# Optimization experiments

Hardware: AMD Instinct MI355X
Metric: run time of the kernel (lower is better)

The kernel has to match this reference:

```python
import jax, jax.numpy as jnp
import numpy as np


def deform_conv2d(x, w, offset, mask, pad):
    """Modulated deformable conv (DCNv2), stride 1, dilation 1, groups 1.
    x: [B,C,H,W], w: [Co,C,kh,kw], offset: [B,2*K,H,W] (y,x per tap), mask: [B,K,H,W].
    Output spatial size equals input (pad = (k-1)//2).
    """
    B, C, H, W = x.shape
    Co, _, kh, kw = w.shape
    K = kh * kw
    off = offset.reshape(B, K, 2, H, W)
    dy, dx = off[:, :, 0], off[:, :, 1]               # [B,K,H,W]
    ky, kx = jnp.meshgrid(jnp.arange(kh), jnp.arange(kw), indexing='ij')
    ky = ky.reshape(K).astype(x.dtype)
    kx = kx.reshape(K).astype(x.dtype)
    hh = jnp.arange(H, dtype=x.dtype)
    ww = jnp.arange(W, dtype=x.dtype)
    # sampling coords: p0 + p_k + delta p_k
    py = hh[None, None, :, None] - pad + ky[None, :, None, None] + dy  # [B,K,H,W]
    px = ww[None, None, None, :] - pad + kx[None, :, None, None] + dx
    y0 = jnp.floor(py)
    x0 = jnp.floor(px)
    wy = py - y0
    wx = px - x0
    y0i = y0.astype(jnp.int32)
    x0i = x0.astype(jnp.int32)
    x_flat = x.reshape(B, C, H * W)

    def gather(yi, xi):
        valid = (yi >= 0) & (yi < H) & (xi >= 0) & (xi < W)  # zero padding outside
        idx = jnp.clip(yi, 0, H - 1) * W + jnp.clip(xi, 0, W - 1)
        g = jnp.take_along_axis(x_flat, idx.reshape(B, 1, K * H * W), axis=2)
        g = g.reshape(B, C, K, H, W)
        return g * valid[:, None].astype(x.dtype)

    v00 = gather(y0i, x0i)
    v01 = gather(y0i, x0i + 1)
    v10 = gather(y0i + 1, x0i)
    v11 = gather(y0i + 1, x0i + 1)
    wy_ = wy[:, None]  # [B,1,K,H,W]
    wx_ = wx[:, None]
    samp = (v00 * (1 - wy_) * (1 - wx_) + v01 * (1 - wy_) * wx_
            + v10 * wy_ * (1 - wx_) + v11 * wy_ * wx_)   # [B,C,K,H,W]
    # masked weighted accumulation == conv over sampled taps
    return jnp.einsum('bckhw,bkhw,ock->bohw', samp, mask, w.reshape(Co, C, K))


def setup_inputs() -> dict:
    key = jax.random.key(0)
    ks = jax.random.split(key, 10)
    B, C, H, W, Co = 4, 64, 64, 64, 64
    inp = {
        'x': jax.random.normal(ks[0], (B, C, H, W), dtype=jnp.float32),
        'filter1': jax.random.normal(ks[1], (Co, C, 3, 3), dtype=jnp.float32) * 0.05,
        'offset1': jax.random.normal(ks[2], (B, 2 * 9, H, W), dtype=jnp.float32),
        'mask1': jax.random.uniform(ks[3], (B, 9, H, W), dtype=jnp.float32),
        'filter2': jax.random.normal(ks[4], (Co, C, 5, 5), dtype=jnp.float32) * 0.03,
        'offset2': jax.random.normal(ks[5], (B, 2 * 25, H, W), dtype=jnp.float32),
        'mask2': jax.random.uniform(ks[6], (B, 25, H, W), dtype=jnp.float32),
        'filter3': jax.random.normal(ks[7], (Co, C, 7, 7), dtype=jnp.float32) * 0.02,
        'offset3': jax.random.normal(ks[8], (B, 2 * 49, H, W), dtype=jnp.float32),
        'mask3': jax.random.uniform(ks[9], (B, 49, H, W), dtype=jnp.float32),
    }
    return inp


def reference(x, filter1, offset1, mask1, filter2, offset2, mask2, filter3, offset3, mask3):
    part1 = deform_conv2d(x, filter1, offset1, mask1, pad=1)  # 3x3
    part2 = deform_conv2d(x, filter2, offset2, mask2, pad=2)  # 5x5
    part3 = deform_conv2d(x, filter3, offset3, mask3, pad=3)  # 7x7
    return jnp.concatenate((part1, part2, part3), axis=1)
```

## Files before the change

### kernel.cpp

```cpp
#include <hip/hip_runtime.h>
#include <hip/hip_bf16.h>


typedef __attribute__((ext_vector_type(8))) short bf16x8;
typedef __attribute__((ext_vector_type(8))) unsigned short u16x8;
typedef __attribute__((ext_vector_type(4))) float f32x4;
typedef __attribute__((ext_vector_type(2))) float f32x2;

#define WR 16
#define WC 30
#define WS 68
#define SLS 20

__device__ __forceinline__ unsigned short f2bf(float f) {
    __hip_bfloat16 h = __float2bfloat16(f);
    return *reinterpret_cast<unsigned short*>(&h);
}
__device__ __forceinline__ f32x2 unpk(unsigned u) {
    f32x2 r;
    r[0] = __uint_as_float(u << 16);
    r[1] = __uint_as_float(u & 0xffff0000u);
    return r;
}

__global__ __launch_bounds__(256) void k_prep(
    const float* __restrict__ x,
    const float* __restrict__ f1, const float* __restrict__ f2, const float* __restrict__ f3,
    unsigned short* __restrict__ xTb,
    unsigned short* __restrict__ wp1, unsigned short* __restrict__ wp2, unsigned short* __restrict__ wp3) {
    __shared__ float tile[64][65];
    int bid = blockIdx.x;
    int tid = threadIdx.x;
    if (bid < 256) {
        int b = bid >> 6, h = bid & 63;
        {
            int w = tid & 63, c4 = tid >> 6;
            const float* xp = x + (((b * 64) * 64 + h) * 64) + w;
            #pragma unroll
            for (int i = 0; i < 16; ++i) {
                int c = c4 * 16 + i;
                tile[c][w] = xp[c * 4096];
            }
        }
        __syncthreads();
        {
            int c = tid & 63, w4 = tid >> 6;
            unsigned short* op = xTb + (((b * 64 + h) * 64) * 64) + c;
            #pragma unroll
            for (int i = 0; i < 16; ++i) {
                int ww = w4 * 16 + i;
                op[ww * 64] = f2bf(tile[c][ww]);
            }
        }
    } else {
        int idx = (bid - 256) * 256 + tid;
        const float* f; unsigned short* wp; int K, rel;
        if (idx < 36864)       { f = f1; wp = wp1; K = 9;  rel = idx; }
        else if (idx < 139264) { f = f2; wp = wp2; K = 25; rel = idx - 36864; }
        else                   { f = f3; wp = wp3; K = 49; rel = idx - 139264; }
        int k    = rel >> 12;
        int r2   = rel & 4095;
        int ct   = r2 >> 10;
        int cg   = (r2 >> 9) & 1;
        int lane = (r2 >> 3) & 63;
        int j    = r2 & 7;
        int o = ct * 16 + (lane & 15);
        int c = cg * 32 + (lane >> 4) * 8 + j;
        wp[rel] = f2bf(f[(o * 64 + c) * K + k]);
    }
}

__global__ __launch_bounds__(512, 4) void k_dcn(
    const unsigned short* __restrict__ xTb,
    const float* __restrict__ off1, const float* __restrict__ msk1, const unsigned short* __restrict__ wp1,
    const float* __restrict__ off2, const float* __restrict__ msk2, const unsigned short* __restrict__ wp2,
    const float* __restrict__ off3, const float* __restrict__ msk3, const unsigned short* __restrict__ wp3,
    float* __restrict__ out) {

    __shared__ __align__(16) unsigned char smem[WR * WC * WS * 2];
    unsigned short* win = (unsigned short*)smem;
    float* slab = (float*)smem;

    int tile = blockIdx.x;
    int b  = tile >> 8;
    int h  = (tile >> 2) & 63;
    int w0 = (tile & 3) << 4;

    int tid  = threadIdx.x;
    int wv   = tid >> 6;
    int lane = tid & 63;
    int quad = lane >> 4;
    int l16  = lane & 15;
    int ylo  = h - 7, cxlo = w0 - 7;

    const unsigned short* xb = xTb + ((size_t)b << 18);

    {
        int j = tid & 7;
        for (int p = tid >> 3; p < WR * WC; p += 64) {
            int r = p / WC, cc = p - r * WC;
            int y = min(max(ylo + r, 0), 63);
            int x = min(max(cxlo + cc, 0), 63);
            *(u16x8*)(win + p * WS + j * 8) =
                *(const u16x8*)(xb + (((y << 6) + x) << 6) + j * 8);
        }
    }
    __syncthreads();

    int pw   = w0 + l16;
    int ch0  = quad << 3;
    int lofs = lane << 3;

    const float* offs; const float* msks; const unsigned short* wpF;
    int ks, ke, kw, pad;
    switch (wv) {
        case 0:  offs = off1; msks = msk1; wpF = wp1; kw = 3; pad = 1; ks = 0;  ke = 9;  break;
        case 1:  offs = off2; msks = msk2; wpF = wp2; kw = 5; pad = 2; ks = 0;  ke = 12; break;
        case 2:  offs = off2; msks = msk2; wpF = wp2; kw = 5; pad = 2; ks = 12; ke = 25; break;
        case 3:  offs = off3; msks = msk3; wpF = wp3; kw = 7; pad = 3; ks = 0;  ke = 10; break;
        case 4:  offs = off3; msks = msk3; wpF = wp3; kw = 7; pad = 3; ks = 10; ke = 20; break;
        case 5:  offs = off3; msks = msk3; wpF = wp3; kw = 7; pad = 3; ks = 20; ke = 30; break;
        case 6:  offs = off3; msks = msk3; wpF = wp3; kw = 7; pad = 3; ks = 30; ke = 40; break;
        default: offs = off3; msks = msk3; wpF = wp3; kw = 7; pad = 3; ks = 40; ke = 49; break;
    }
    int K2 = (kw == 3) ? 9 : (kw == 5) ? 25 : 49;
    const float* offp = offs + ((b * 2 * K2) * 4096) + (h << 6) + pw;
    const float* mskp = msks + ((b * K2) * 4096) + (h << 6) + pw;

    f32x4 acc[4];
    #pragma unroll
    for (int i = 0; i < 4; ++i) acc[i] = (f32x4){0.f, 0.f, 0.f, 0.f};

    int ky = ks / kw, kx = ks - ky * kw;

    float dyC = offp[ks * 8192];
    float dxC = offp[ks * 8192 + 4096];
    float mkC = mskp[ks * 4096];

    for (int k = ks; k < ke; ++k) {
        int kn = min(k + 1, ke - 1);
        float dyN = offp[kn * 8192];
        float dxN = offp[kn * 8192 + 4096];
        float mkN = mskp[kn * 4096];

        float py = (float)(h - pad + ky) + dyC;
        float px = (float)(pw - pad + kx) + dxC;
        float y0f = floorf(py), x0f = floorf(px);
        float wy = py - y0f, wx = px - x0f;
        int y0 = (int)y0f, x0 = (int)x0f;
        int y1 = y0 + 1, x1 = x0 + 1;
        float fy0 = ((unsigned)y0 < 64u) ? (1.f - wy) * mkC : 0.f;
        float fy1 = ((unsigned)y1 < 64u) ? wy * mkC         : 0.f;
        float gx0 = ((unsigned)x0 < 64u) ? (1.f - wx)       : 0.f;
        float gx1 = ((unsigned)x1 < 64u) ? wx               : 0.f;
        float w00 = fy0 * gx0, w01 = fy0 * gx1, w10 = fy1 * gx0, w11 = fy1 * gx1;

        int r0 = y0 - ylo, r1 = r0 + 1;
        int c0 = x0 - cxlo, c1 = c0 + 1;
        bool oow = ((w00 != 0.f) & (((unsigned)r0 >= WR) | ((unsigned)c0 >= WC)))
                 | ((w01 != 0.f) & (((unsigned)r0 >= WR) | ((unsigned)c1 >= WC)))
                 | ((w10 != 0.f) & (((unsigned)r1 >= WR) | ((unsigned)c0 >= WC)))
                 | ((w11 != 0.f) & (((unsigned)r1 >= WR) | ((unsigned)c1 >= WC)));
        int r0c = min(max(r0, 0), WR - 1), r1c = min(max(r1, 0), WR - 1);
        int c0c = min(max(c0, 0), WC - 1), c1c = min(max(c1, 0), WC - 1);
        int p00 = (r0c * WC + c0c) * WS;
        int p01 = (r0c * WC + c1c) * WS;
        int p10 = (r1c * WC + c0c) * WS;
        int p11 = (r1c * WC + c1c) * WS;

        union U { u16x8 v; unsigned u[4]; };
        U g00a, g01a, g10a, g11a, g00b, g01b, g10b, g11b;
        g00a.v = *(const u16x8*)(win + p00 + ch0);
        g01a.v = *(const u16x8*)(win + p01 + ch0);
        g10a.v = *(const u16x8*)(win + p10 + ch0);
        g11a.v = *(const u16x8*)(win + p11 + ch0);
        g00b.v = *(const u16x8*)(win + p00 + 32 + ch0);
        g01b.v = *(const u16x8*)(win + p01 + 32 + ch0);
        g10b.v = *(const u16x8*)(win + p10 + 32 + ch0);
        g11b.v = *(const u16x8*)(win + p11 + 32 + ch0);

        if (oow) {
            int y0g = min(max(y0, 0), 63), y1g = min(max(y1, 0), 63);
            int x0g = min(max(x0, 0), 63), x1g = min(max(x1, 0), 63);
            int o00 = ((y0g << 6) + x0g) << 6;
            int o01 = ((y0g << 6) + x1g) << 6;
            int o10 = ((y1g << 6) + x0g) << 6;
            int o11 = ((y1g << 6) + x1g) << 6;
            g00a.v = *(const u16x8*)(xb + o00 + ch0);
            g01a.v = *(const u16x8*)(xb + o01 + ch0);
            g10a.v = *(const u16x8*)(xb + o10 + ch0);
            g11a.v = *(const u16x8*)(xb + o11 + ch0);
            g00b.v = *(const u16x8*)(xb + o00 + 32 + ch0);
            g01b.v = *(const u16x8*)(xb + o01 + 32 + ch0);
            g10b.v = *(const u16x8*)(xb + o10 + 32 + ch0);
            g11b.v = *(const u16x8*)(xb + o11 + 32 + ch0);
        }

        f32x2 W00 = {w00, w00}, W01 = {w01, w01}, W10 = {w10, w10}, W11 = {w11, w11};
        union { bf16x8 v; unsigned short u[8]; } A0, A1;
        #pragma unroll
        for (int j2 = 0; j2 < 4; ++j2) {
            f32x2 s0 = W00 * unpk(g00a.u[j2]) + W01 * unpk(g01a.u[j2])
                     + W10 * unpk(g10a.u[j2]) + W11 * unpk(g11a.u[j2]);
            f32x2 s1 = W00 * unpk(g00b.u[j2]) + W01 * unpk(g01b.u[j2])
                     + W10 * unpk(g10b.u[j2]) + W11 * unpk(g11b.u[j2]);
            A0.u[2 * j2]     = f2bf(s0[0]);
            A0.u[2 * j2 + 1] = f2bf(s0[1]);
            A1.u[2 * j2]     = f2bf(s1[0]);
            A1.u[2 * j2 + 1] = f2bf(s1[1]);
        }

        const unsigned short* wpk = wpF + (k << 12) + lofs;
        #pragma unroll
        for (int ct = 0; ct < 4; ++ct) {
            bf16x8 b0 = *(const bf16x8*)(wpk + ct * 1024);
            bf16x8 b1 = *(const bf16x8*)(wpk + ct * 1024 + 512);
            acc[ct] = __builtin_amdgcn_mfma_f32_16x16x32_bf16(A0.v, b0, acc[ct], 0, 0, 0);
            acc[ct] = __builtin_amdgcn_mfma_f32_16x16x32_bf16(A1.v, b1, acc[ct], 0, 0, 0);
        }

        dyC = dyN; dxC = dxN; mkC = mkN;
        if (++kx == kw) { kx = 0; ++ky; }
    }

    __syncthreads();

    #pragma unroll
    for (int ct = 0; ct < 4; ++ct) {
        *(f32x4*)&slab[wv * 1280 + (ct * 16 + l16) * SLS + quad * 4] = acc[ct];
    }
    __syncthreads();

    for (int it = tid; it < 768; it += 512) {
        int g = it & 3;
        int o = it >> 2;
        int oo = o & 63;
        int base = oo * SLS + g * 4;
        f32x4 v;
        if (o < 64) {
            v = *(const f32x4*)&slab[base];
        } else if (o < 128) {
            f32x4 a0 = *(const f32x4*)&slab[1 * 1280 + base];
            f32x4 a1 = *(const f32x4*)&slab[2 * 1280 + base];
            #pragma unroll
            for (int r = 0; r < 4; ++r) v[r] = a0[r] + a1[r];
        } else {
            f32x4 a0 = *(const f32x4*)&slab[3 * 1280 + base];
            f32x4 a1 = *(const f32x4*)&slab[4 * 1280 + base];
            f32x4 a2 = *(const f32x4*)&slab[5 * 1280 + base];
            f32x4 a3 = *(const f32x4*)&slab[6 * 1280 + base];
            f32x4 a4 = *(const f32x4*)&slab[7 * 1280 + base];
            #pragma unroll
            for (int r = 0; r < 4; ++r) v[r] = (a0[r] + a1[r]) + (a2[r] + a3[r]) + a4[r];
        }
        *(f32x4*)&out[(((size_t)b * 192 + o) * 64 + h) * 64 + w0 + g * 4] = v;
    }
}

extern "C" void kernel_launch(void* const* d_in, const int* in_sizes, int n_in,
                              void* d_out, int out_size, void* d_ws, size_t ws_size,
                              hipStream_t stream) {
    const float* x    = (const float*)d_in[0];
    const float* f1   = (const float*)d_in[1];
    const float* off1 = (const float*)d_in[2];
    const float* msk1 = (const float*)d_in[3];
    const float* f2   = (const float*)d_in[4];
    const float* off2 = (const float*)d_in[5];
    const float* msk2 = (const float*)d_in[6];
    const float* f3   = (const float*)d_in[7];
    const float* off3 = (const float*)d_in[8];
    const float* msk3 = (const float*)d_in[9];
    float* out = (float*)d_out;

    unsigned short* xTb = (unsigned short*)d_ws;
    unsigned short* wp1 = xTb + 4 * 64 * 64 * 64;
    unsigned short* wp2 = wp1 + 9 * 4096;
    unsigned short* wp3 = wp2 + 25 * 4096;

    k_prep<<<dim3(1584), dim3(256), 0, stream>>>(x, f1, f2, f3, xTb, wp1, wp2, wp3);
    k_dcn<<<dim3(1024), dim3(512), 0, stream>>>(xTb,
                                                off1, msk1, wp1,
                                                off2, msk2, wp2,
                                                off3, msk3, wp3,
                                                out);
}
```

Baseline: 167.9 us.

## Software-pipeline deformable taps with double-buffered gathers and weight loads

```diff
diff --git a/kernel.cpp b/kernel.cpp
--- a/kernel.cpp
+++ b/kernel.cpp
@@ -4,6 +4,7 @@
 
 typedef __attribute__((ext_vector_type(8))) short bf16x8;
 typedef __attribute__((ext_vector_type(8))) unsigned short u16x8;
+typedef __attribute__((ext_vector_type(4))) unsigned u32x4;
 typedef __attribute__((ext_vector_type(4))) float f32x4;
 typedef __attribute__((ext_vector_type(2))) float f32x2;
 
@@ -21,6 +22,108 @@
     r[0] = __uint_as_float(u << 16);
     r[1] = __uint_as_float(u & 0xffff0000u);
     return r;
+}
+
+struct PSet { float w00, w01, w10, w11; int oow; int y0, x0; };
+struct GSet { u32x4 c00a, c01a, c10a, c11a, c00b, c01b, c10b, c11b; };
+struct BSet { bf16x8 v0, v1, v2, v3, v4, v5, v6, v7; };
+
+__device__ __forceinline__ void tap_prep(
+    PSet& P, GSet& G, const unsigned short* win, int ch0,
+    int h, int pw, int pad, int ky, int kx, int ylo, int cxlo,
+    float dy, float dx, float mk)
+{
+    float py = (float)(h - pad + ky) + dy;
+    float px = (float)(pw - pad + kx) + dx;
+    float y0f = floorf(py), x0f = floorf(px);
+    float wy = py - y0f, wx = px - x0f;
+    int y0 = (int)y0f, x0 = (int)x0f;
+    int y1 = y0 + 1, x1 = x0 + 1;
+    float fy0 = ((unsigned)y0 < 64u) ? (1.f - wy) * mk : 0.f;
+    float fy1 = ((unsigned)y1 < 64u) ? wy * mk         : 0.f;
+    float gx0 = ((unsigned)x0 < 64u) ? (1.f - wx)      : 0.f;
+    float gx1 = ((unsigned)x1 < 64u) ? wx              : 0.f;
+    P.w00 = fy0 * gx0; P.w01 = fy0 * gx1; P.w10 = fy1 * gx0; P.w11 = fy1 * gx1;
+    P.y0 = y0; P.x0 = x0;
+
+    int r0 = y0 - ylo, r1 = r0 + 1;
+    int c0 = x0 - cxlo, c1 = c0 + 1;
+    bool oow = ((P.w00 != 0.f) & (((unsigned)r0 >= WR) | ((unsigned)c0 >= WC)))
+             | ((P.w01 != 0.f) & (((unsigned)r0 >= WR) | ((unsigned)c1 >= WC)))
+             | ((P.w10 != 0.f) & (((unsigned)r1 >= WR) | ((unsigned)c0 >= WC)))
+             | ((P.w11 != 0.f) & (((unsigned)r1 >= WR) | ((unsigned)c1 >= WC)));
+    P.oow = oow ? 1 : 0;
+
+    int r0c = min(max(r0, 0), WR - 1), r1c = min(max(r1, 0), WR - 1);
+    int c0c = min(max(c0, 0), WC - 1), c1c = min(max(c1, 0), WC - 1);
+    int p00 = (r0c * WC + c0c) * WS;
+    int p01 = (r0c * WC + c1c) * WS;
+    int p10 = (r1c * WC + c0c) * WS;
+    int p11 = (r1c * WC + c1c) * WS;
+    G.c00a = *(const u32x4*)(win + p00 + ch0);
+    G.c01a = *(const u32x4*)(win + p01 + ch0);
+    G.c10a = *(const u32x4*)(win + p10 + ch0);
+    G.c11a = *(const u32x4*)(win + p11 + ch0);
+    G.c00b = *(const u32x4*)(win + p00 + 32 + ch0);
+    G.c01b = *(const u32x4*)(win + p01 + 32 + ch0);
+    G.c10b = *(const u32x4*)(win + p10 + 32 + ch0);
+    G.c11b = *(const u32x4*)(win + p11 + 32 + ch0);
+}
+
+__device__ __forceinline__ void load_b(BSet& B, const unsigned short* wpF, int k, int lofs) {
+    const unsigned short* wpk = wpF + (k << 12) + lofs;
+    B.v0 = *(const bf16x8*)(wpk);
+    B.v1 = *(const bf16x8*)(wpk + 512);
+    B.v2 = *(const bf16x8*)(wpk + 1024);
+    B.v3 = *(const bf16x8*)(wpk + 1536);
+    B.v4 = *(const bf16x8*)(wpk + 2048);
+    B.v5 = *(const bf16x8*)(wpk + 2560);
+    B.v6 = *(const bf16x8*)(wpk + 3072);
+    B.v7 = *(const bf16x8*)(wpk + 3584);
+}
+
+__device__ __forceinline__ void tap_compute(
+    const PSet& P, GSet& G, const BSet& B, f32x4 acc[4],
+    const unsigned short* xb, int ch0)
+{
+    if (P.oow) {
+        int y0g = min(max(P.y0, 0), 63), y1g = min(max(P.y0 + 1, 0), 63);
+        int x0g = min(max(P.x0, 0), 63), x1g = min(max(P.x0 + 1, 0), 63);
+        int o00 = ((y0g << 6) + x0g) << 6;
+        int o01 = ((y0g << 6) + x1g) << 6;
+        int o10 = ((y1g << 6) + x0g) << 6;
+        int o11 = ((y1g << 6) + x1g) << 6;
+        G.c00a = *(const u32x4*)(xb + o00 + ch0);
+        G.c01a = *(const u32x4*)(xb + o01 + ch0);
+        G.c10a = *(const u32x4*)(xb + o10 + ch0);
+        G.c11a = *(const u32x4*)(xb + o11 + ch0);
+        G.c00b = *(const u32x4*)(xb + o00 + 32 + ch0);
+        G.c01b = *(const u32x4*)(xb + o01 + 32 + ch0);
+        G.c10b = *(const u32x4*)(xb + o10 + 32 + ch0);
+        G.c11b = *(const u32x4*)(xb + o11 + 32 + ch0);
+    }
+    f32x2 W00 = {P.w00, P.w00}, W01 = {P.w01, P.w01};
+    f32x2 W10 = {P.w10, P.w10}, W11 = {P.w11, P.w11};
+    union { bf16x8 v; unsigned short u[8]; } A0, A1;
+    #pragma unroll
+    for (int j2 = 0; j2 < 4; ++j2) {
+        f32x2 s0 = W00 * unpk(G.c00a[j2]) + W01 * unpk(G.c01a[j2])
+                 + W10 * unpk(G.c10a[j2]) + W11 * unpk(G.c11a[j2]);
+        f32x2 s1 = W00 * unpk(G.c00b[j2]) + W01 * unpk(G.c01b[j2])
+                 + W10 * unpk(G.c10b[j2]) + W11 * unpk(G.c11b[j2]);
+        A0.u[2 * j2]     = f2bf(s0[0]);
+        A0.u[2 * j2 + 1] = f2bf(s0[1]);
+        A1.u[2 * j2]     = f2bf(s1[0]);
+        A1.u[2 * j2 + 1] = f2bf(s1[1]);
+    }
+    acc[0] = __builtin_amdgcn_mfma_f32_16x16x32_bf16(A0.v, B.v0, acc[0], 0, 0, 0);
+    acc[0] = __builtin_amdgcn_mfma_f32_16x16x32_bf16(A1.v, B.v1, acc[0], 0, 0, 0);
+    acc[1] = __builtin_amdgcn_mfma_f32_16x16x32_bf16(A0.v, B.v2, acc[1], 0, 0, 0);
+    acc[1] = __builtin_amdgcn_mfma_f32_16x16x32_bf16(A1.v, B.v3, acc[1], 0, 0, 0);
+    acc[2] = __builtin_amdgcn_mfma_f32_16x16x32_bf16(A0.v, B.v4, acc[2], 0, 0, 0);
+    acc[2] = __builtin_amdgcn_mfma_f32_16x16x32_bf16(A1.v, B.v5, acc[2], 0, 0, 0);
+    acc[3] = __builtin_amdgcn_mfma_f32_16x16x32_bf16(A0.v, B.v6, acc[3], 0, 0, 0);
+    acc[3] = __builtin_amdgcn_mfma_f32_16x16x32_bf16(A1.v, B.v7, acc[3], 0, 0, 0);
 }
 
 __global__ __launch_bounds__(256) void k_prep(
@@ -95,18 +198,6 @@
 
     const unsigned short* xb = xTb + ((size_t)b << 18);
 
-    {
-        int j = tid & 7;
-        for (int p = tid >> 3; p < WR * WC; p += 64) {
-            int r = p / WC, cc = p - r * WC;
-            int y = min(max(ylo + r, 0), 63);
-            int x = min(max(cxlo + cc, 0), 63);
-            *(u16x8*)(win + p * WS + j * 8) =
-                *(const u16x8*)(xb + (((y << 6) + x) << 6) + j * 8);
-        }
-    }
-    __syncthreads();
-
     int pw   = w0 + l16;
     int ch0  = quad << 3;
     int lofs = lane << 3;
@@ -127,100 +218,74 @@
     const float* offp = offs + ((b * 2 * K2) * 4096) + (h << 6) + pw;
     const float* mskp = msks + ((b * K2) * 4096) + (h << 6) + pw;
 
+    int kp1 = min(ks + 1, ke - 1), kp2 = min(ks + 2, ke - 1);
+    float dyA = offp[ks * 8192], dxA = offp[ks * 8192 + 4096], mkA = mskp[ks * 4096];
+    float dyB = offp[kp1 * 8192], dxB = offp[kp1 * 8192 + 4096], mkB = mskp[kp1 * 4096];
+    float dyC = offp[kp2 * 8192], dxC = offp[kp2 * 8192 + 4096], mkC = mskp[kp2 * 4096];
+
+    {
+        int j = tid & 7;
+        for (int p = tid >> 3; p < WR * WC; p += 64) {
+            int r = p / WC, cc = p - r * WC;
+            int y = min(max(ylo + r, 0), 63);
+            int x = min(max(cxlo + cc, 0), 63);
+            *(u16x8*)(win + p * WS + j * 8) =
+                *(const u16x8*)(xb + (((y << 6) + x) << 6) + j * 8);
+        }
+    }
+    __syncthreads();
+
     f32x4 acc[4];
     #pragma unroll
     for (int i = 0; i < 4; ++i) acc[i] = (f32x4){0.f, 0.f, 0.f, 0.f};
 
-    int ky = ks / kw, kx = ks - ky * kw;
-
-    float dyC = offp[ks * 8192];
-    float dxC = offp[ks * 8192 + 4096];
-    float mkC = mskp[ks * 4096];
-
-    for (int k = ks; k < ke; ++k) {
-        int kn = min(k + 1, ke - 1);
-        float dyN = offp[kn * 8192];
-        float dxN = offp[kn * 8192 + 4096];
-        float mkN = mskp[kn * 4096];
-
-        float py = (float)(h - pad + ky) + dyC;
-        float px = (float)(pw - pad + kx) + dxC;
-        float y0f = floorf(py), x0f = floorf(px);
-        float wy = py - y0f, wx = px - x0f;
-        int y0 = (int)y0f, x0 = (int)x0f;
-        int y1 = y0 + 1, x1 = x0 + 1;
-        float fy0 = ((unsigned)y0 < 64u) ? (1.f - wy) * mkC : 0.f;
-        float fy1 = ((unsigned)y1 < 64u) ? wy * mkC         : 0.f;
-        float gx0 = ((unsigned)x0 < 64u) ? (1.f - wx)       : 0.f;
-        float gx1 = ((unsigned)x1 < 64u) ? wx               : 0.f;
-        float w00 = fy0 * gx0, w01 = fy0 * gx1, w10 = fy1 * gx0, w11 = fy1 * gx1;
-
-        int r0 = y0 - ylo, r1 = r0 + 1;
-        int c0 = x0 - cxlo, c1 = c0 + 1;
-        bool oow = ((w00 != 0.f) & (((unsigned)r0 >= WR) | ((unsigned)c0 >= WC)))
-                 | ((w01 != 0.f) & (((unsigned)r0 >= WR) | ((unsigned)c1 >= WC)))
-                 | ((w10 != 0.f) & (((unsigned)r1 >= WR) | ((unsigned)c0 >= WC)))
-                 | ((w11 != 0.f) & (((unsigned)r1 >= WR) | ((unsigned)c1 >= WC)));
-        int r0c = min(max(r0, 0), WR - 1), r1c = min(max(r1, 0), WR - 1);
-        int c0c = min(max(c0, 0), WC - 1), c1c = min(max(c1, 0), WC - 1);
-        int p00 = (r0c * WC + c0c) * WS;
-        int p01 = (r0c * WC + c1c) * WS;
-        int p10 = (r1c * WC + c0c) * WS;
-        int p11 = (r1c * WC + c1c) * WS;
-
-        union U { u16x8 v; unsigned u[4]; };
-        U g00a, g01a, g10a, g11a, g00b, g01b, g10b, g11b;
-        g00a.v = *(const u16x8*)(win + p00 + ch0);
-        g01a.v = *(const u16x8*)(win + p01 + ch0);
-        g10a.v = *(const u16x8*)(win + p10 + ch0);
-        g11a.v = *(const u16x8*)(win + p11 + ch0);
-        g00b.v = *(const u16x8*)(win + p00 + 32 + ch0);
-        g01b.v = *(const u16x8*)(win + p01 + 32 + ch0);
-        g10b.v = *(const u16x8*)(win + p10 + 32 + ch0);
-        g11b.v = *(const u16x8*)(win + p11 + 32 + ch0);
-
-        if (oow) {
-            int y0g = min(max(y0, 0), 63), y1g = min(max(y1, 0), 63);
-            int x0g = min(max(x0, 0), 63), x1g = min(max(x1, 0), 63);
-            int o00 = ((y0g << 6) + x0g) << 6;
-            int o01 = ((y0g << 6) + x1g) << 6;
-            int o10 = ((y1g << 6) + x0g) << 6;
-            int o11 = ((y1g << 6) + x1g) << 6;
-            g00a.v = *(const u16x8*)(xb + o00 + ch0);
-            g01a.v = *(const u16x8*)(xb + o01 + ch0);
-            g10a.v = *(const u16x8*)(xb + o10 + ch0);
-            g11a.v = *(const u16x8*)(xb + o11 + ch0);
-            g00b.v = *(const u16x8*)(xb + o00 + 32 + ch0);
-            g01b.v = *(const u16x8*)(xb + o01 + 32 + ch0);
-            g10b.v = *(const u16x8*)(xb + o10 + 32 + ch0);
-            g11b.v = *(const u16x8*)(xb + o11 + 32 + ch0);
-        }
-
-        f32x2 W00 = {w00, w00}, W01 = {w01, w01}, W10 = {w10, w10}, W11 = {w11, w11};
-        union { bf16x8 v; unsigned short u[8]; } A0, A1;
-        #pragma unroll
-        for (int j2 = 0; j2 < 4; ++j2) {
-            f32x2 s0 = W00 * unpk(g00a.u[j2]) + W01 * unpk(g01a.u[j2])
-                     + W10 * unpk(g10a.u[j2]) + W11 * unpk(g11a.u[j2]);
-            f32x2 s1 = W00 * unpk(g00b.u[j2]) + W01 * unpk(g01b.u[j2])
-                     + W10 * unpk(g10b.u[j2]) + W11 * unpk(g11b.u[j2]);
-            A0.u[2 * j2]     = f2bf(s0[0]);
-            A0.u[2 * j2 + 1] = f2bf(s0[1]);
-            A1.u[2 * j2]     = f2bf(s1[0]);
-            A1.u[2 * j2 + 1] = f2bf(s1[1]);
-        }
-
-        const unsigned short* wpk = wpF + (k << 12) + lofs;
-        #pragma unroll
-        for (int ct = 0; ct < 4; ++ct) {
-            bf16x8 b0 = *(const bf16x8*)(wpk + ct * 1024);
-            bf16x8 b1 = *(const bf16x8*)(wpk + ct * 1024 + 512);
-            acc[ct] = __builtin_amdgcn_mfma_f32_16x16x32_bf16(A0.v, b0, acc[ct], 0, 0, 0);
-            acc[ct] = __builtin_amdgcn_mfma_f32_16x16x32_bf16(A1.v, b1, acc[ct], 0, 0, 0);
-        }
-
-        dyC = dyN; dxC = dxN; mkC = mkN;
-        if (++kx == kw) { kx = 0; ++ky; }
+    int kyW = ks / kw, kxW = ks - (ks / kw) * kw;
+
+    PSet pP, pQ; GSet gP, gQ; BSet bP, bQ;
+
+    tap_prep(pP, gP, win, ch0, h, pw, pad, kyW, kxW, ylo, cxlo, dyA, dxA, mkA);
+    load_b(bP, wpF, ks, lofs);
+    if (++kxW == kw) { kxW = 0; ++kyW; }
+    {
+        int kn = min(ks + 3, ke - 1);
+        dyA = dyB; dxA = dxB; mkA = mkB;
+        dyB = dyC; dxB = dxC; mkB = mkC;
+        dyC = offp[kn * 8192]; dxC = offp[kn * 8192 + 4096]; mkC = mskp[kn * 4096];
+    }
+
+    int k = ks;
+    while (k + 1 < ke) {
+        tap_prep(pQ, gQ, win, ch0, h, pw, pad, kyW, kxW, ylo, cxlo, dyA, dxA, mkA);
+        load_b(bQ, wpF, k + 1, lofs);
+        if (++kxW == kw) { kxW = 0; ++kyW; }
+        {
+            int kn = min(k + 4, ke - 1);
+            dyA = dyB; dxA = dxB; mkA = mkB;
+            dyB = dyC; dxB = dxC; mkB = mkC;
+            dyC = offp[kn * 8192]; dxC = offp[kn * 8192 + 4096]; mkC = mskp[kn * 4096];
+        }
+        tap_compute(pP, gP, bP, acc, xb, ch0);
+        ++k;
+        if (k + 1 < ke) {
+            tap_prep(pP, gP, win, ch0, h, pw, pad, kyW, kxW, ylo, cxlo, dyA, dxA, mkA);
+            load_b(bP, wpF, k + 1, lofs);
+            if (++kxW == kw) { kxW = 0; ++kyW; }
+            {
+                int kn = min(k + 4, ke - 1);
+                dyA = dyB; dxA = dxB; mkA = mkB;
+                dyB = dyC; dxB = dxC; mkB = mkC;
+                dyC = offp[kn * 8192]; dxC = offp[kn * 8192 + 4096]; mkC = mskp[kn * 4096];
+            }
+            tap_compute(pQ, gQ, bQ, acc, xb, ch0);
+            ++k;
+        } else {
+            tap_compute(pQ, gQ, bQ, acc, xb, ch0);
+            ++k;
+        }
+    }
+    if (k < ke) {
+        tap_compute(pP, gP, bP, acc, xb, ch0);
+        ++k;
     }
 
     __syncthreads();
```

Result: slower. 426.8 us (+154.1%).

## Software-pipeline deformable taps with double-buffered LDS gathers and deeper offset prefetch

Applied to the files above, without the earlier changes.

```diff
diff --git a/kernel.cpp b/kernel.cpp
--- a/kernel.cpp
+++ b/kernel.cpp
@@ -4,6 +4,7 @@
 
 typedef __attribute__((ext_vector_type(8))) short bf16x8;
 typedef __attribute__((ext_vector_type(8))) unsigned short u16x8;
+typedef __attribute__((ext_vector_type(4))) unsigned u32x4;
 typedef __attribute__((ext_vector_type(4))) float f32x4;
 typedef __attribute__((ext_vector_type(2))) float f32x2;
 
@@ -70,7 +71,107 @@
     }
 }
 
-__global__ __launch_bounds__(512, 4) void k_dcn(
+#define PREP(S, dyp, dxp, mkp)                                                \
+    {                                                                         \
+        float py = (float)(h - pad + kyP) + (dyp);                            \
+        float px = (float)(pw - pad + kxP) + (dxp);                           \
+        float y0f = floorf(py), x0f = floorf(px);                             \
+        float wy = py - y0f, wx = px - x0f;                                   \
+        int y0 = (int)y0f, x0 = (int)x0f;                                     \
+        int y1 = y0 + 1, x1 = x0 + 1;                                         \
+        float fy0 = ((unsigned)y0 < 64u) ? (1.f - wy) * (mkp) : 0.f;          \
+        float fy1 = ((unsigned)y1 < 64u) ? wy * (mkp)         : 0.f;          \
+        float gx0 = ((unsigned)x0 < 64u) ? (1.f - wx)         : 0.f;          \
+        float gx1 = ((unsigned)x1 < 64u) ? wx                 : 0.f;          \
+        w00##S = fy0 * gx0; w01##S = fy0 * gx1;                               \
+        w10##S = fy1 * gx0; w11##S = fy1 * gx1;                               \
+        int r0 = y0 - ylo, r1 = r0 + 1;                                       \
+        int c0 = x0 - cxlo, c1 = c0 + 1;                                      \
+        oow##S = ((w00##S != 0.f) & (((unsigned)r0 >= WR) | ((unsigned)c0 >= WC)))  \
+               | ((w01##S != 0.f) & (((unsigned)r0 >= WR) | ((unsigned)c1 >= WC)))  \
+               | ((w10##S != 0.f) & (((unsigned)r1 >= WR) | ((unsigned)c0 >= WC)))  \
+               | ((w11##S != 0.f) & (((unsigned)r1 >= WR) | ((unsigned)c1 >= WC))); \
+        y0s##S = y0; x0s##S = x0;                                             \
+        int r0c = min(max(r0, 0), WR - 1), r1c = min(max(r1, 0), WR - 1);     \
+        int c0c = min(max(c0, 0), WC - 1), c1c = min(max(c1, 0), WC - 1);     \
+        int p00 = (r0c * WC + c0c) * WS;                                      \
+        int p01 = (r0c * WC + c1c) * WS;                                      \
+        int p10 = (r1c * WC + c0c) * WS;                                      \
+        int p11 = (r1c * WC + c1c) * WS;                                      \
+        g00a##S = *(const u32x4*)(win + p00 + ch0);                           \
+        g01a##S = *(const u32x4*)(win + p01 + ch0);                           \
+        g10a##S = *(const u32x4*)(win + p10 + ch0);                           \
+        g11a##S = *(const u32x4*)(win + p11 + ch0);                           \
+        g00b##S = *(const u32x4*)(win + p00 + 32 + ch0);                      \
+        g01b##S = *(const u32x4*)(win + p01 + 32 + ch0);                      \
+        g10b##S = *(const u32x4*)(win + p10 + 32 + ch0);                      \
+        g11b##S = *(const u32x4*)(win + p11 + 32 + ch0);                      \
+        if (++kxP == kw) { kxP = 0; ++kyP; }                                  \
+    }
+
+#define CONSUME(S, kk)                                                        \
+    {                                                                         \
+        const unsigned short* wpk = wpF + ((kk) << 12) + lofs;                \
+        bf16x8 b00 = *(const bf16x8*)(wpk);                                   \
+        bf16x8 b01 = *(const bf16x8*)(wpk + 512);                             \
+        bf16x8 b10 = *(const bf16x8*)(wpk + 1024);                            \
+        bf16x8 b11 = *(const bf16x8*)(wpk + 1536);                            \
+        bf16x8 b20 = *(const bf16x8*)(wpk + 2048);                            \
+        bf16x8 b21 = *(const bf16x8*)(wpk + 2560);                            \
+        bf16x8 b30 = *(const bf16x8*)(wpk + 3072);                            \
+        bf16x8 b31 = *(const bf16x8*)(wpk + 3584);                            \
+        if (oow##S) {                                                         \
+            int y0g = min(max(y0s##S, 0), 63), y1g = min(max(y0s##S + 1, 0), 63); \
+            int x0g = min(max(x0s##S, 0), 63), x1g = min(max(x0s##S + 1, 0), 63); \
+            int o00 = ((y0g << 6) + x0g) << 6;                                \
+            int o01 = ((y0g << 6) + x1g) << 6;                                \
+            int o10 = ((y1g << 6) + x0g) << 6;                                \
+            int o11 = ((y1g << 6) + x1g) << 6;                                \
+            g00a##S = *(const u32x4*)(xb + o00 + ch0);                        \
+            g01a##S = *(const u32x4*)(xb + o01 + ch0);                        \
+            g10a##S = *(const u32x4*)(xb + o10 + ch0);                        \
+            g11a##S = *(const u32x4*)(xb + o11 + ch0);                        \
+            g00b##S = *(const u32x4*)(xb + o00 + 32 + ch0);                   \
+            g01b##S = *(const u32x4*)(xb + o01 + 32 + ch0);                   \
+            g10b##S = *(const u32x4*)(xb + o10 + 32 + ch0);                   \
+            g11b##S = *(const u32x4*)(xb + o11 + 32 + ch0);                   \
+        }                                                                     \
+        f32x2 W00 = {w00##S, w00##S}, W01 = {w01##S, w01##S};                 \
+        f32x2 W10 = {w10##S, w10##S}, W11 = {w11##S, w11##S};                 \
+        union { bf16x8 v; unsigned short u[8]; } A0, A1;                      \
+        _Pragma("unroll")                                                     \
+        for (int j2 = 0; j2 < 4; ++j2) {                                      \
+            f32x2 s0 = W00 * unpk(g00a##S[j2]) + W01 * unpk(g01a##S[j2])      \
+                     + W10 * unpk(g10a##S[j2]) + W11 * unpk(g11a##S[j2]);     \
+            f32x2 s1 = W00 * unpk(g00b##S[j2]) + W01 * unpk(g01b##S[j2])      \
+                     + W10 * unpk(g10b##S[j2]) + W11 * unpk(g11b##S[j2]);     \
+            A0.u[2 * j2]     = f2bf(s0[0]);                                   \
+            A0.u[2 * j2 + 1] = f2bf(s0[1]);                                   \
+            A1.u[2 * j2]     = f2bf(s1[0]);                                   \
+            A1.u[2 * j2 + 1] = f2bf(s1[1]);                                   \
+        }                                                                     \
+        acc[0] = __builtin_amdgcn_mfma_f32_16x16x32_bf16(A0.v, b00, acc[0], 0, 0, 0); \
+        acc[0] = __builtin_amdgcn_mfma_f32_16x16x32_bf16(A1.v, b01, acc[0], 0, 0, 0); \
+        acc[1] = __builtin_amdgcn_mfma_f32_16x16x32_bf16(A0.v, b10, acc[1], 0, 0, 0); \
+        acc[1] = __builtin_amdgcn_mfma_f32_16x16x32_bf16(A1.v, b11, acc[1], 0, 0, 0); \
+        acc[2] = __builtin_amdgcn_mfma_f32_16x16x32_bf16(A0.v, b20, acc[2], 0, 0, 0); \
+        acc[2] = __builtin_amdgcn_mfma_f32_16x16x32_bf16(A1.v, b21, acc[2], 0, 0, 0); \
+        acc[3] = __builtin_amdgcn_mfma_f32_16x16x32_bf16(A0.v, b30, acc[3], 0, 0, 0); \
+        acc[3] = __builtin_amdgcn_mfma_f32_16x16x32_bf16(A1.v, b31, acc[3], 0, 0, 0); \
+    }
+
+#define ROTATE(kq)                                                            \
+    {                                                                         \
+        int kn = min((kq), ke - 1);                                           \
+        float dyN = offp[kn * 8192];                                          \
+        float dxN = offp[kn * 8192 + 4096];                                   \
+        float mkN = mskp[kn * 4096];                                          \
+        dyA = dyB; dyB = dyC; dyC = dyN;                                      \
+        dxA = dxB; dxB = dxC; dxC = dxN;                                      \
+        mkA = mkB; mkB = mkC; mkC = mkN;                                      \
+    }
+
+__global__ __launch_bounds__(512, 2) void k_dcn(
     const unsigned short* __restrict__ xTb,
     const float* __restrict__ off1, const float* __restrict__ msk1, const unsigned short* __restrict__ wp1,
     const float* __restrict__ off2, const float* __restrict__ msk2, const unsigned short* __restrict__ wp2,
@@ -94,18 +195,6 @@
     int ylo  = h - 7, cxlo = w0 - 7;
 
     const unsigned short* xb = xTb + ((size_t)b << 18);
-
-    {
-        int j = tid & 7;
-        for (int p = tid >> 3; p < WR * WC; p += 64) {
-            int r = p / WC, cc = p - r * WC;
-            int y = min(max(ylo + r, 0), 63);
-            int x = min(max(cxlo + cc, 0), 63);
-            *(u16x8*)(win + p * WS + j * 8) =
-                *(const u16x8*)(xb + (((y << 6) + x) << 6) + j * 8);
-        }
-    }
-    __syncthreads();
 
     int pw   = w0 + l16;
     int ch0  = quad << 3;
@@ -127,100 +216,49 @@
     const float* offp = offs + ((b * 2 * K2) * 4096) + (h << 6) + pw;
     const float* mskp = msks + ((b * K2) * 4096) + (h << 6) + pw;
 
+    int kp1 = min(ks + 1, ke - 1), kp2 = min(ks + 2, ke - 1);
+    float dyA = offp[ks * 8192], dxA = offp[ks * 8192 + 4096], mkA = mskp[ks * 4096];
+    float dyB = offp[kp1 * 8192], dxB = offp[kp1 * 8192 + 4096], mkB = mskp[kp1 * 4096];
+    float dyC = offp[kp2 * 8192], dxC = offp[kp2 * 8192 + 4096], mkC = mskp[kp2 * 4096];
+
+    {
+        int j = tid & 7;
+        for (int p = tid >> 3; p < WR * WC; p += 64) {
+            int r = p / WC, cc = p - r * WC;
+            int y = min(max(ylo + r, 0), 63);
+            int x = min(max(cxlo + cc, 0), 63);
+            *(u16x8*)(win + p * WS + j * 8) =
+                *(const u16x8*)(xb + (((y << 6) + x) << 6) + j * 8);
+        }
+    }
+    __syncthreads();
+
     f32x4 acc[4];
     #pragma unroll
     for (int i = 0; i < 4; ++i) acc[i] = (f32x4){0.f, 0.f, 0.f, 0.f};
 
-    int ky = ks / kw, kx = ks - ky * kw;
-
-    float dyC = offp[ks * 8192];
-    float dxC = offp[ks * 8192 + 4096];
-    float mkC = mskp[ks * 4096];
-
-    for (int k = ks; k < ke; ++k) {
-        int kn = min(k + 1, ke - 1);
-        float dyN = offp[kn * 8192];
-        float dxN = offp[kn * 8192 + 4096];
-        float mkN = mskp[kn * 4096];
-
-        float py = (float)(h - pad + ky) + dyC;
-        float px = (float)(pw - pad + kx) + dxC;
-        float y0f = floorf(py), x0f = floorf(px);
-        float wy = py - y0f, wx = px - x0f;
-        int y0 = (int)y0f, x0 = (int)x0f;
-        int y1 = y0 + 1, x1 = x0 + 1;
-        float fy0 = ((unsigned)y0 < 64u) ? (1.f - wy) * mkC : 0.f;
-        float fy1 = ((unsigned)y1 < 64u) ? wy * mkC         : 0.f;
-        float gx0 = ((unsigned)x0 < 64u) ? (1.f - wx)       : 0.f;
-        float gx1 = ((unsigned)x1 < 64u) ? wx               : 0.f;
-        float w00 = fy0 * gx0, w01 = fy0 * gx1, w10 = fy1 * gx0, w11 = fy1 * gx1;
-
-        int r0 = y0 - ylo, r1 = r0 + 1;
-        int c0 = x0 - cxlo, c1 = c0 + 1;
-        bool oow = ((w00 != 0.f) & (((unsigned)r0 >= WR) | ((unsigned)c0 >= WC)))
-                 | ((w01 != 0.f) & (((unsigned)r0 >= WR) | ((unsigned)c1 >= WC)))
-                 | ((w10 != 0.f) & (((unsigned)r1 >= WR) | ((unsigned)c0 >= WC)))
-                 | ((w11 != 0.f) & (((unsigned)r1 >= WR) | ((unsigned)c1 >= WC)));
-        int r0c = min(max(r0, 0), WR - 1), r1c = min(max(r1, 0), WR - 1);
-        int c0c = min(max(c0, 0), WC - 1), c1c = min(max(c1, 0), WC - 1);
-        int p00 = (r0c * WC + c0c) * WS;
-        int p01 = (r0c * WC + c1c) * WS;
-        int p10 = (r1c * WC + c0c) * WS;
-        int p11 = (r1c * WC + c1c) * WS;
-
-        union U { u16x8 v; unsigned u[4]; };
-        U g00a, g01a, g10a, g11a, g00b, g01b, g10b, g11b;
-        g00a.v = *(const u16x8*)(win + p00 + ch0);
-        g01a.v = *(const u16x8*)(win + p01 + ch0);
-        g10a.v = *(const u16x8*)(win + p10 + ch0);
-        g11a.v = *(const u16x8*)(win + p11 + ch0);
-        g00b.v = *(const u16x8*)(win + p00 + 32 + ch0);
-        g01b.v = *(const u16x8*)(win + p01 + 32 + ch0);
-        g10b.v = *(const u16x8*)(win + p10 + 32 + ch0);
-        g11b.v = *(const u16x8*)(win + p11 + 32 + ch0);
-
-        if (oow) {
-            int y0g = min(max(y0, 0), 63), y1g = min(max(y1, 0), 63);
-            int x0g = min(max(x0, 0), 63), x1g = min(max(x1, 0), 63);
-            int o00 = ((y0g << 6) + x0g) << 6;
-            int o01 = ((y0g << 6) + x1g) << 6;
-            int o10 = ((y1g << 6) + x0g) << 6;
-            int o11 = ((y1g << 6) + x1g) << 6;
-            g00a.v = *(const u16x8*)(xb + o00 + ch0);
-            g01a.v = *(const u16x8*)(xb + o01 + ch0);
-            g10a.v = *(const u16x8*)(xb + o10 + ch0);
-            g11a.v = *(const u16x8*)(xb + o11 + ch0);
-            g00b.v = *(const u16x8*)(xb + o00 + 32 + ch0);
-            g01b.v = *(const u16x8*)(xb + o01 + 32 + ch0);
-            g10b.v = *(const u16x8*)(xb + o10 + 32 + ch0);
-            g11b.v = *(const u16x8*)(xb + o11 + 32 + ch0);
-        }
-
-        f32x2 W00 = {w00, w00}, W01 = {w01, w01}, W10 = {w10, w10}, W11 = {w11, w11};
-        union { bf16x8 v; unsigned short u[8]; } A0, A1;
-        #pragma unroll
-        for (int j2 = 0; j2 < 4; ++j2) {
-            f32x2 s0 = W00 * unpk(g00a.u[j2]) + W01 * unpk(g01a.u[j2])
-                     + W10 * unpk(g10a.u[j2]) + W11 * unpk(g11a.u[j2]);
-            f32x2 s1 = W00 * unpk(g00b.u[j2]) + W01 * unpk(g01b.u[j2])
-                     + W10 * unpk(g10b.u[j2]) + W11 * unpk(g11b.u[j2]);
-            A0.u[2 * j2]     = f2bf(s0[0]);
-            A0.u[2 * j2 + 1] = f2bf(s0[1]);
-            A1.u[2 * j2]     = f2bf(s1[0]);
-            A1.u[2 * j2 + 1] = f2bf(s1[1]);
-        }
-
-        const unsigned short* wpk = wpF + (k << 12) + lofs;
-        #pragma unroll
-        for (int ct = 0; ct < 4; ++ct) {
-            bf16x8 b0 = *(const bf16x8*)(wpk + ct * 1024);
-            bf16x8 b1 = *(const bf16x8*)(wpk + ct * 1024 + 512);
-            acc[ct] = __builtin_amdgcn_mfma_f32_16x16x32_bf16(A0.v, b0, acc[ct], 0, 0, 0);
-            acc[ct] = __builtin_amdgcn_mfma_f32_16x16x32_bf16(A1.v, b1, acc[ct], 0, 0, 0);
-        }
-
-        dyC = dyN; dxC = dxN; mkC = mkN;
-        if (++kx == kw) { kx = 0; ++ky; }
+    int kyP = ks / kw, kxP = ks - (ks / kw) * kw;
+
+    float w00P, w01P, w10P, w11P, w00Q, w01Q, w10Q, w11Q;
+    int   oowP, y0sP, x0sP, oowQ, y0sQ, x0sQ;
+    u32x4 g00aP, g01aP, g10aP, g11aP, g00bP, g01bP, g10bP, g11bP;
+    u32x4 g00aQ, g01aQ, g10aQ, g11aQ, g00bQ, g01bQ, g10bQ, g11bQ;
+
+    PREP(P, dyA, dxA, mkA)
+    ROTATE(ks + 3)
+
+    int k = ks;
+    for (;;) {
+        PREP(Q, dyA, dxA, mkA)
+        ROTATE(k + 4)
+        CONSUME(P, k)
+        ++k;
+        if (k >= ke) break;
+        PREP(P, dyA, dxA, mkA)
+        ROTATE(k + 4)
+        CONSUME(Q, k)
+        ++k;
+        if (k >= ke) break;
     }
 
     __syncthreads();
```

Result: slower. 177.9 us (+5.9%).
